# Kernel tuning notes

Measured on AMD Instinct MI355X. Metric: run time of the kernel, lower is better.

## Reference

```python
import jax, jax.numpy as jnp
import numpy as np

EMBED = 1024
HEAD = 64

def setup_inputs() -> dict:
    key = jax.random.key(0)
    k1, k2, k3, k4 = jax.random.split(key, 4)
    embeddings = jax.random.normal(k1, (8, 2048, EMBED), dtype=jnp.float32)
    # nn.Linear weight is [out, in]; we store transposed [in, out] for x @ W
    scale = 1.0 / np.sqrt(EMBED)
    Wk = jax.random.uniform(k2, (EMBED, HEAD), dtype=jnp.float32, minval=-scale, maxval=scale)
    Wq = jax.random.uniform(k3, (EMBED, HEAD), dtype=jnp.float32, minval=-scale, maxval=scale)
    Wv = jax.random.uniform(k4, (EMBED, HEAD), dtype=jnp.float32, minval=-scale, maxval=scale)
    return {"embeddings": embeddings, "Wq": Wq, "Wk": Wk, "Wv": Wv}

def reference(embeddings, Wq, Wk, Wv):
    B, S, D = embeddings.shape
    q = embeddings @ Wq  # [B,S,H]
    k = embeddings @ Wk
    v = embeddings @ Wv
    norm = k.shape[-1] ** (-0.5)
    scores = jnp.einsum('bqh,bkh->bqk', q, k) * norm  # [B,S,S]
    causal = jnp.tril(jnp.ones((S, S), dtype=bool))
    scores = jnp.where(causal, scores, -jnp.inf)
    weights = jax.nn.softmax(scores, axis=-1)
    # dropout p=0.0 (eval-equivalent): identity
    return jnp.einsum('bqk,bkh->bqh', weights, v)
```

## Files before the change

### kernel.cpp

```cpp
#include <hip/hip_runtime.h>

#define SEQ   2048
#define NBATCH 8
#define EMB   1024
#define HD    64
#define QKVSZ (NBATCH * SEQ * HD)
#define WTSZ  (3 * HD * EMB)
#define PSLOT 1088

typedef __attribute__((ext_vector_type(8))) short bf16x8;
typedef __attribute__((ext_vector_type(4))) float f32x4;

__device__ inline unsigned short f2b(float f) {
  union { float f; unsigned int i; } u; u.f = f;
  unsigned int r = (u.i + 0x7FFFu + ((u.i >> 16) & 1u)) >> 16;
  return (unsigned short)r;
}

__global__ __launch_bounds__(256) void wtrans_kernel(const float* __restrict__ wq,
                                                     const float* __restrict__ wk,
                                                     const float* __restrict__ wv,
                                                     unsigned short* __restrict__ wt) {
  int i = blockIdx.x * 256 + threadIdx.x;
  int kb  = i / 12288;
  int rem = i - kb * 12288;
  int m   = rem >> 12;
  int c   = (rem >> 6) & 63;
  int kd  = rem & 63;
  const float* src = (m == 0) ? wq : ((m == 1) ? wk : wv);
  int d = kb * 64 + kd;
  wt[i] = f2b(src[d * 64 + c]);
}

__global__ __launch_bounds__(256, 4) void qkv_proj_kernel(const float* __restrict__ emb,
                                                          const unsigned short* __restrict__ wt,
                                                          unsigned short* __restrict__ qkv) {
  __shared__ __align__(16) unsigned short Ab[2][32 * 64];
  __shared__ __align__(16) unsigned short Wb[2][96 * 64];

  const int t    = threadIdx.x;
  const int wave = t >> 6;
  const int lane = t & 63;
  const int quad = lane >> 4;
  const int l16  = lane & 15;
  const int bx = blockIdx.x;
  const int rt = bx >> 1;
  const int ch = bx & 1;
  const int wr = wave >> 1;
  const int wc = wave & 1;

  const float* aBase = emb + (size_t)rt * 32 * EMB;
  const unsigned short* wBase = wt + ch * 6144;

  f32x4 acc[3];
#pragma unroll
  for (int j = 0; j < 3; j++) acc[j] = (f32x4){0.f, 0.f, 0.f, 0.f};

  f32x4 pa[2];
  bf16x8 pw[3];

#pragma unroll
  for (int j = 0; j < 2; j++) {
    int u = t + j * 256;
    pa[j] = *(const f32x4*)(aBase + (size_t)(u >> 4) * EMB + (u & 15) * 4);
  }
#pragma unroll
  for (int j = 0; j < 3; j++) {
    int u = t + j * 256;
    pw[j] = *(const bf16x8*)(wBase + u * 8);
  }
#pragma unroll
  for (int j = 0; j < 2; j++) {
    int u = t + j * 256;
    int row = u >> 4, kq = u & 15;
    unsigned int lo = (unsigned int)f2b(pa[j][0]) | ((unsigned int)f2b(pa[j][1]) << 16);
    unsigned int hi = (unsigned int)f2b(pa[j][2]) | ((unsigned int)f2b(pa[j][3]) << 16);
    uint2 pk; pk.x = lo; pk.y = hi;
    *(uint2*)((char*)&Ab[0][0] + row * 128 + ((kq * 8) ^ ((row & 7) << 4))) = pk;
  }
#pragma unroll
  for (int j = 0; j < 3; j++) {
    int u = t + j * 256;
    int coll = u >> 3, kd8 = u & 7;
    *(bf16x8*)((char*)&Wb[0][0] + coll * 128 + ((kd8 ^ (coll & 7)) << 4)) = pw[j];
  }
  __syncthreads();

#pragma unroll 2
  for (int kb = 0; kb < 16; kb++) {
    const int cur = kb & 1;

    if (kb < 15) {
#pragma unroll
      for (int j = 0; j < 2; j++) {
        int u = t + j * 256;
        pa[j] = *(const f32x4*)(aBase + (size_t)(u >> 4) * EMB + (kb + 1) * 64 + (u & 15) * 4);
      }
#pragma unroll
      for (int j = 0; j < 3; j++) {
        int u = t + j * 256;
        pw[j] = *(const bf16x8*)(wBase + (kb + 1) * 12288 + u * 8);
      }
    }

    const int arow = wr * 16 + l16;
#pragma unroll
    for (int kh = 0; kh < 2; kh++) {
      bf16x8 af = *(const bf16x8*)((const char*)&Ab[cur][0] + arow * 128 +
                                   ((kh * 64 + quad * 16) ^ ((arow & 7) << 4)));
#pragma unroll
      for (int j = 0; j < 3; j++) {
        const int coll = (wc * 3 + j) * 16 + l16;
        bf16x8 wf = *(const bf16x8*)((const char*)&Wb[cur][0] + coll * 128 +
                                     ((kh * 64 + quad * 16) ^ ((coll & 7) << 4)));
        acc[j] = __builtin_amdgcn_mfma_f32_16x16x32_bf16(af, wf, acc[j], 0, 0, 0);
      }
    }

    if (kb < 15) {
      const int nb = cur ^ 1;
#pragma unroll
      for (int j = 0; j < 2; j++) {
        int u = t + j * 256;
        int row = u >> 4, kq = u & 15;
        unsigned int lo = (unsigned int)f2b(pa[j][0]) | ((unsigned int)f2b(pa[j][1]) << 16);
        unsigned int hi = (unsigned int)f2b(pa[j][2]) | ((unsigned int)f2b(pa[j][3]) << 16);
        uint2 pk; pk.x = lo; pk.y = hi;
        *(uint2*)((char*)&Ab[nb][0] + row * 128 + ((kq * 8) ^ ((row & 7) << 4))) = pk;
      }
#pragma unroll
      for (int j = 0; j < 3; j++) {
        int u = t + j * 256;
        int coll = u >> 3, kd8 = u & 7;
        *(bf16x8*)((char*)&Wb[nb][0] + coll * 128 + ((kd8 ^ (coll & 7)) << 4)) = pw[j];
      }
      __syncthreads();
    }
  }

#pragma unroll
  for (int j = 0; j < 3; j++) {
    int gc = ch * 96 + (wc * 3 + j) * 16 + l16;
    if (gc < 128) {
      int m  = gc >> 6, cm = gc & 63;
#pragma unroll
      for (int r = 0; r < 4; r++) {
        int row = rt * 32 + wr * 16 + quad * 4 + r;
        qkv[(size_t)m * QKVSZ + (size_t)row * HD + cm] = f2b(acc[j][r]);
      }
    }
  }

  if (ch == 1) {
    __syncthreads();
    unsigned short* Vsh = (unsigned short*)&Ab[0][0];
#pragma unroll
    for (int j = 0; j < 3; j++) {
      int gc = 96 + (wc * 3 + j) * 16 + l16;
      if (gc >= 128) {
        int h = gc - 128;
#pragma unroll
        for (int r = 0; r < 4; r++)
          Vsh[h * 40 + wr * 16 + quad * 4 + r] = f2b(acc[j][r]);
      }
    }
    __syncthreads();
    int h  = t >> 2;
    int sq = (t & 3) * 8;
    int row0 = rt * 32;
    int b    = row0 >> 11;
    int seq0 = row0 & 2047;
    bf16x8 vv = *(const bf16x8*)(Vsh + h * 40 + sq);
    *(bf16x8*)(qkv + 2 * (size_t)QKVSZ + ((size_t)(b * 64 + h)) * SEQ + seq0 + sq) = vv;
  }
}

__global__ __launch_bounds__(64, 2) void attn_split(const unsigned short* __restrict__ qkv,
                                                    float* __restrict__ part,
                                                    float* __restrict__ out) {
  __shared__ __align__(16) unsigned short Ksh[64 * 64];
  __shared__ __align__(16) unsigned short Vt[64 * 64];
  __shared__ __align__(16) unsigned short Psh[16 * 64];

  const int t = threadIdx.x;
  const int quad = t >> 4;
  const int l16  = t & 15;
  const int idx = blockIdx.x;
  const int b   = blockIdx.y;
  const int qt  = (idx < 128) ? idx : (idx - 64);
  const int c   = (idx < 128) ? 0 : 1;
  const int q0  = qt * 16;
  const int kdiag = qt >> 2;
  int t0, t1;
  if (qt < 64) { t0 = 0; t1 = kdiag; }
  else {
    int n0 = (kdiag + 2) >> 1;
    t0 = c ? n0 : 0;
    t1 = c ? kdiag : (n0 - 1);
  }

  const unsigned short* qg = qkv;
  const unsigned short* kg = qkv + QKVSZ;
  const unsigned short* vg = qkv + 2 * QKVSZ;

  const unsigned short* qptr = qg + ((size_t)(b * SEQ + q0 + l16)) * HD + quad * 8;
  const bf16x8 qf0 = *(const bf16x8*)qptr;
  const bf16x8 qf1 = *(const bf16x8*)(qptr + 32);

  f32x4 o0 = {0,0,0,0}, o1 = {0,0,0,0}, o2 = {0,0,0,0}, o3 = {0,0,0,0};
  float mst[4] = {-INFINITY, -INFINITY, -INFINITY, -INFINITY};
  float lst[4] = {0.f, 0.f, 0.f, 0.f};
  const float sc = 0.125f * 1.44269504088896f;

  bf16x8 kpre[8], vpre[8];
  {
    const unsigned short* kgb = kg + ((size_t)(b * SEQ + t0 * 64)) * HD;
#pragma unroll
    for (int i = 0; i < 8; i++) {
      int u = t + i * 64;
      kpre[i] = *(const bf16x8*)(kgb + (size_t)(u >> 3) * HD + (u & 7) * 8);
      vpre[i] = *(const bf16x8*)(vg + ((size_t)(b * 64 + (u >> 3))) * SEQ + t0 * 64 + (u & 7) * 8);
    }
  }

  for (int kb = t0; kb <= t1; kb++) {
#pragma unroll
    for (int i = 0; i < 8; i++) {
      int u = t + i * 64;
      int row = u >> 3, sb = (u & 7) * 16;
      *(bf16x8*)((char*)Ksh + row * 128 + (sb ^ ((row & 7) << 4))) = kpre[i];
      *(bf16x8*)((char*)Vt  + row * 128 + (sb ^ ((row & 7) << 4))) = vpre[i];
    }
    __syncthreads();

    if (kb < t1) {
      const unsigned short* kgb = kg + ((size_t)(b * SEQ + (kb + 1) * 64)) * HD;
#pragma unroll
      for (int i = 0; i < 8; i++) {
        int u = t + i * 64;
        kpre[i] = *(const bf16x8*)(kgb + (size_t)(u >> 3) * HD + (u & 7) * 8);
        vpre[i] = *(const bf16x8*)(vg + ((size_t)(b * 64 + (u >> 3))) * SEQ + (kb + 1) * 64 + (u & 7) * 8);
      }
    }

    f32x4 s[4];
#pragma unroll
    for (int kt = 0; kt < 4; kt++) {
      int row = kt * 16 + l16;
      bf16x8 kf0 = *(const bf16x8*)((char*)Ksh + row * 128 + ((quad * 16) ^ ((row & 7) << 4)));
      bf16x8 kf1 = *(const bf16x8*)((char*)Ksh + row * 128 + ((64 + quad * 16) ^ ((row & 7) << 4)));
      f32x4 z = {0.f, 0.f, 0.f, 0.f};
      z = __builtin_amdgcn_mfma_f32_16x16x32_bf16(qf0, kf0, z, 0, 0, 0);
      z = __builtin_amdgcn_mfma_f32_16x16x32_bf16(qf1, kf1, z, 0, 0, 0);
      s[kt] = z;
    }

    if (kb == kdiag) {
#pragma unroll
      for (int r = 0; r < 4; r++) {
        int rowg = q0 + quad * 4 + r;
#pragma unroll
        for (int kt = 0; kt < 4; kt++) {
          int col = kb * 64 + kt * 16 + l16;
          float v = s[kt][r] * sc;
          s[kt][r] = (col > rowg) ? -INFINITY : v;
        }
      }
    } else {
#pragma unroll
      for (int r = 0; r < 4; r++)
#pragma unroll
        for (int kt = 0; kt < 4; kt++) s[kt][r] *= sc;
    }

    float alpha[4];
#pragma unroll
    for (int r = 0; r < 4; r++) {
      float mx = fmaxf(fmaxf(s[0][r], s[1][r]), fmaxf(s[2][r], s[3][r]));
#pragma unroll
      for (int off = 1; off < 16; off <<= 1) mx = fmaxf(mx, __shfl_xor(mx, off, 64));
      float mnew = fmaxf(mst[r], mx);
      alpha[r] = exp2f(mst[r] - mnew);
      mst[r] = mnew;
    }
#pragma unroll
    for (int r = 0; r < 4; r++) {
      float sm = 0.f;
#pragma unroll
      for (int kt = 0; kt < 4; kt++) {
        float p = exp2f(s[kt][r] - mst[r]);
        s[kt][r] = p;
        sm += p;
      }
#pragma unroll
      for (int off = 1; off < 16; off <<= 1) sm += __shfl_xor(sm, off, 64);
      lst[r] = lst[r] * alpha[r] + sm;
    }
#pragma unroll
    for (int r = 0; r < 4; r++) { o0[r] *= alpha[r]; o1[r] *= alpha[r]; o2[r] *= alpha[r]; o3[r] *= alpha[r]; }

#pragma unroll
    for (int kt = 0; kt < 4; kt++)
#pragma unroll
      for (int r = 0; r < 4; r++) {
        int row = quad * 4 + r;
        *(unsigned short*)((char*)Psh + row * 128 + ((kt * 32 + l16 * 2) ^ ((row & 7) << 4))) = f2b(s[kt][r]);
      }
    __syncthreads();

#pragma unroll
    for (int kc = 0; kc < 2; kc++) {
      bf16x8 pf = *(const bf16x8*)((char*)Psh + l16 * 128 + ((kc * 64 + quad * 16) ^ ((l16 & 7) << 4)));
#pragma unroll
      for (int ht = 0; ht < 1; ht++) {}
      {
        int r0 = 0 * 16 + l16, r1 = 1 * 16 + l16, r2 = 2 * 16 + l16, r3 = 3 * 16 + l16;
        bf16x8 vf0 = *(const bf16x8*)((char*)Vt + r0 * 128 + ((kc * 64 + quad * 16) ^ ((r0 & 7) << 4)));
        bf16x8 vf1 = *(const bf16x8*)((char*)Vt + r1 * 128 + ((kc * 64 + quad * 16) ^ ((r1 & 7) << 4)));
        bf16x8 vf2 = *(const bf16x8*)((char*)Vt + r2 * 128 + ((kc * 64 + quad * 16) ^ ((r2 & 7) << 4)));
        bf16x8 vf3 = *(const bf16x8*)((char*)Vt + r3 * 128 + ((kc * 64 + quad * 16) ^ ((r3 & 7) << 4)));
        o0 = __builtin_amdgcn_mfma_f32_16x16x32_bf16(pf, vf0, o0, 0, 0, 0);
        o1 = __builtin_amdgcn_mfma_f32_16x16x32_bf16(pf, vf1, o1, 0, 0, 0);
        o2 = __builtin_amdgcn_mfma_f32_16x16x32_bf16(pf, vf2, o2, 0, 0, 0);
        o3 = __builtin_amdgcn_mfma_f32_16x16x32_bf16(pf, vf3, o3, 0, 0, 0);
      }
    }
    __syncthreads();
  }

  if (qt < 64) {
#pragma unroll
    for (int r = 0; r < 4; r++) {
      float inv = 1.f / lst[r];
      int rowg = q0 + quad * 4 + r;
      size_t ob = ((size_t)(b * SEQ + rowg)) * HD + l16;
      out[ob + 0]  = o0[r] * inv;
      out[ob + 16] = o1[r] * inv;
      out[ob + 32] = o2[r] * inv;
      out[ob + 48] = o3[r] * inv;
    }
  } else {
    float* ps = part + ((size_t)((b * 64 + (qt - 64)) * 2 + c)) * PSLOT;
#pragma unroll
    for (int r = 0; r < 4; r++) {
      int row = quad * 4 + r;
      ps[row * 64 + 0  + l16] = o0[r];
      ps[row * 64 + 16 + l16] = o1[r];
      ps[row * 64 + 32 + l16] = o2[r];
      ps[row * 64 + 48 + l16] = o3[r];
      if (l16 == 0) {
        ps[1024 + row] = mst[r];
        ps[1040 + row] = lst[r];
      }
    }
  }
}

__global__ __launch_bounds__(64) void attn_merge(const float* __restrict__ part,
                                                 float* __restrict__ out) {
  const int h  = threadIdx.x;
  const int qx = blockIdx.x;
  const int b  = blockIdx.y;
  const float* p0 = part + ((size_t)((b * 64 + qx) * 2 + 0)) * PSLOT;
  const float* p1 = p0 + PSLOT;
#pragma unroll 4
  for (int r = 0; r < 16; r++) {
    float m0 = p0[1024 + r], l0 = p0[1040 + r];
    float m1 = p1[1024 + r], l1 = p1[1040 + r];
    float M  = fmaxf(m0, m1);
    float e0 = exp2f(m0 - M), e1 = exp2f(m1 - M);
    float L  = l0 * e0 + l1 * e1;
    float o  = (p0[r * 64 + h] * e0 + p1[r * 64 + h] * e1) / L;
    out[((size_t)(b * SEQ + (64 + qx) * 16 + r)) * HD + h] = o;
  }
}

extern "C" void kernel_launch(void* const* d_in, const int* in_sizes, int n_in,
                              void* d_out, int out_size, void* d_ws, size_t ws_size,
                              hipStream_t stream) {
  const float* emb = (const float*)d_in[0];
  const float* wq  = (const float*)d_in[1];
  const float* wk  = (const float*)d_in[2];
  const float* wv  = (const float*)d_in[3];
  unsigned short* ws  = (unsigned short*)d_ws;
  unsigned short* wt  = ws;
  unsigned short* qkv = ws + WTSZ;
  float* part = (float*)(ws + WTSZ + 3 * QKVSZ);

  hipLaunchKernelGGL(wtrans_kernel,   dim3(WTSZ / 256), dim3(256), 0, stream, wq, wk, wv, wt);
  hipLaunchKernelGGL(qkv_proj_kernel, dim3(1024),       dim3(256), 0, stream, emb, wt, qkv);
  hipLaunchKernelGGL(attn_split,      dim3(192, 8),     dim3(64),  0, stream, qkv, part, (float*)d_out);
  hipLaunchKernelGGL(attn_merge,      dim3(64, 8),      dim3(64),  0, stream, part, (float*)d_out);
}
```

Measured before the change: 161.5 us.

## Share K/V tiles across four waves with double buffering and chunked split-K

Result: slower. 209.0 us (+29.4%).

```diff
diff --git a/kernel.cpp b/kernel.cpp
--- a/kernel.cpp
+++ b/kernel.cpp
@@ -6,7 +6,7 @@
 #define HD    64
 #define QKVSZ (NBATCH * SEQ * HD)
 #define WTSZ  (3 * HD * EMB)
-#define PSLOT 1088
+#define PSLOT2 4224
 
 typedef __attribute__((ext_vector_type(8))) short bf16x8;
 typedef __attribute__((ext_vector_type(4))) float f32x4;
@@ -175,29 +175,27 @@
   }
 }
 
-__global__ __launch_bounds__(64, 2) void attn_split(const unsigned short* __restrict__ qkv,
-                                                    float* __restrict__ part,
-                                                    float* __restrict__ out) {
-  __shared__ __align__(16) unsigned short Ksh[64 * 64];
-  __shared__ __align__(16) unsigned short Vt[64 * 64];
-  __shared__ __align__(16) unsigned short Psh[16 * 64];
-
-  const int t = threadIdx.x;
-  const int quad = t >> 4;
-  const int l16  = t & 15;
-  const int idx = blockIdx.x;
-  const int b   = blockIdx.y;
-  const int qt  = (idx < 128) ? idx : (idx - 64);
-  const int c   = (idx < 128) ? 0 : 1;
-  const int q0  = qt * 16;
-  const int kdiag = qt >> 2;
-  int t0, t1;
-  if (qt < 64) { t0 = 0; t1 = kdiag; }
-  else {
-    int n0 = (kdiag + 2) >> 1;
-    t0 = c ? n0 : 0;
-    t1 = c ? kdiag : (n0 - 1);
-  }
+__global__ __launch_bounds__(256, 4) void attn_split(const unsigned short* __restrict__ qkv,
+                                                     float* __restrict__ part,
+                                                     float* __restrict__ out) {
+  __shared__ __align__(16) unsigned short Kb[2][64 * 64];
+  __shared__ __align__(16) unsigned short Vb[2][64 * 64];
+  __shared__ __align__(16) unsigned short Pb[4][16 * 64];
+
+  const int t    = threadIdx.x;
+  const int wave = t >> 6;
+  const int lane = t & 63;
+  const int quad = lane >> 4;
+  const int l16  = lane & 15;
+  const int B0 = blockIdx.x;
+  const int c  = blockIdx.y;
+  const int b  = blockIdx.z;
+  const int nch = (B0 >> 2) + 1;
+  if (c >= nch) return;
+  const int t0 = c * 4;
+  const int t1 = min(t0 + 3, B0);
+  const int qt = B0 * 4 + wave;
+  const int q0 = qt * 16;
 
   const unsigned short* qg = qkv;
   const unsigned short* kg = qkv + QKVSZ;
@@ -212,33 +210,30 @@
   float lst[4] = {0.f, 0.f, 0.f, 0.f};
   const float sc = 0.125f * 1.44269504088896f;
 
-  bf16x8 kpre[8], vpre[8];
-  {
-    const unsigned short* kgb = kg + ((size_t)(b * SEQ + t0 * 64)) * HD;
-#pragma unroll
-    for (int i = 0; i < 8; i++) {
-      int u = t + i * 64;
-      kpre[i] = *(const bf16x8*)(kgb + (size_t)(u >> 3) * HD + (u & 7) * 8);
-      vpre[i] = *(const bf16x8*)(vg + ((size_t)(b * 64 + (u >> 3))) * SEQ + t0 * 64 + (u & 7) * 8);
-    }
-  }
+  bf16x8 kpre[2], vpre[2];
+#pragma unroll
+  for (int i = 0; i < 2; i++) {
+    int u = t + i * 256;
+    kpre[i] = *(const bf16x8*)(kg + ((size_t)(b * SEQ + t0 * 64 + (u >> 3))) * HD + (u & 7) * 8);
+    vpre[i] = *(const bf16x8*)(vg + ((size_t)(b * 64 + (u >> 3))) * SEQ + t0 * 64 + (u & 7) * 8);
+  }
+#pragma unroll
+  for (int i = 0; i < 2; i++) {
+    int u = t + i * 256;
+    int row = u >> 3, sb = (u & 7) * 16;
+    *(bf16x8*)((char*)&Kb[0][0] + row * 128 + (sb ^ ((row & 7) << 4))) = kpre[i];
+    *(bf16x8*)((char*)&Vb[0][0] + row * 128 + (sb ^ ((row & 7) << 4))) = vpre[i];
+  }
+  __syncthreads();
 
   for (int kb = t0; kb <= t1; kb++) {
-#pragma unroll
-    for (int i = 0; i < 8; i++) {
-      int u = t + i * 64;
-      int row = u >> 3, sb = (u & 7) * 16;
-      *(bf16x8*)((char*)Ksh + row * 128 + (sb ^ ((row & 7) << 4))) = kpre[i];
-      *(bf16x8*)((char*)Vt  + row * 128 + (sb ^ ((row & 7) << 4))) = vpre[i];
-    }
-    __syncthreads();
+    const int cur = (kb - t0) & 1;
 
     if (kb < t1) {
-      const unsigned short* kgb = kg + ((size_t)(b * SEQ + (kb + 1) * 64)) * HD;
-#pragma unroll
-      for (int i = 0; i < 8; i++) {
-        int u = t + i * 64;
-        kpre[i] = *(const bf16x8*)(kgb + (size_t)(u >> 3) * HD + (u & 7) * 8);
+#pragma unroll
+      for (int i = 0; i < 2; i++) {
+        int u = t + i * 256;
+        kpre[i] = *(const bf16x8*)(kg + ((size_t)(b * SEQ + (kb + 1) * 64 + (u >> 3))) * HD + (u & 7) * 8);
         vpre[i] = *(const bf16x8*)(vg + ((size_t)(b * 64 + (u >> 3))) * SEQ + (kb + 1) * 64 + (u & 7) * 8);
       }
     }
@@ -247,15 +242,15 @@
 #pragma unroll
     for (int kt = 0; kt < 4; kt++) {
       int row = kt * 16 + l16;
-      bf16x8 kf0 = *(const bf16x8*)((char*)Ksh + row * 128 + ((quad * 16) ^ ((row & 7) << 4)));
-      bf16x8 kf1 = *(const bf16x8*)((char*)Ksh + row * 128 + ((64 + quad * 16) ^ ((row & 7) << 4)));
+      bf16x8 kf0 = *(const bf16x8*)((char*)&Kb[cur][0] + row * 128 + ((quad * 16) ^ ((row & 7) << 4)));
+      bf16x8 kf1 = *(const bf16x8*)((char*)&Kb[cur][0] + row * 128 + ((64 + quad * 16) ^ ((row & 7) << 4)));
       f32x4 z = {0.f, 0.f, 0.f, 0.f};
       z = __builtin_amdgcn_mfma_f32_16x16x32_bf16(qf0, kf0, z, 0, 0, 0);
       z = __builtin_amdgcn_mfma_f32_16x16x32_bf16(qf1, kf1, z, 0, 0, 0);
       s[kt] = z;
     }
 
-    if (kb == kdiag) {
+    if (kb == B0) {
 #pragma unroll
       for (int r = 0; r < 4; r++) {
         int rowg = q0 + quad * 4 + r;
@@ -304,31 +299,39 @@
 #pragma unroll
       for (int r = 0; r < 4; r++) {
         int row = quad * 4 + r;
-        *(unsigned short*)((char*)Psh + row * 128 + ((kt * 32 + l16 * 2) ^ ((row & 7) << 4))) = f2b(s[kt][r]);
-      }
+        *(unsigned short*)((char*)&Pb[wave][0] + row * 128 +
+                           ((kt * 32 + l16 * 2) ^ ((row & 7) << 4))) = f2b(s[kt][r]);
+      }
+
+#pragma unroll
+    for (int kc = 0; kc < 2; kc++) {
+      bf16x8 pf = *(const bf16x8*)((char*)&Pb[wave][0] + l16 * 128 +
+                                   ((kc * 64 + quad * 16) ^ ((l16 & 7) << 4)));
+      int r0 = l16, r1 = 16 + l16, r2 = 32 + l16, r3 = 48 + l16;
+      bf16x8 vf0 = *(const bf16x8*)((char*)&Vb[cur][0] + r0 * 128 + ((kc * 64 + quad * 16) ^ ((r0 & 7) << 4)));
+      bf16x8 vf1 = *(const bf16x8*)((char*)&Vb[cur][0] + r1 * 128 + ((kc * 64 + quad * 16) ^ ((r1 & 7) << 4)));
+      bf16x8 vf2 = *(const bf16x8*)((char*)&Vb[cur][0] + r2 * 128 + ((kc * 64 + quad * 16) ^ ((r2 & 7) << 4)));
+      bf16x8 vf3 = *(const bf16x8*)((char*)&Vb[cur][0] + r3 * 128 + ((kc * 64 + quad * 16) ^ ((r3 & 7) << 4)));
+      o0 = __builtin_amdgcn_mfma_f32_16x16x32_bf16(pf, vf0, o0, 0, 0, 0);
+      o1 = __builtin_amdgcn_mfma_f32_16x16x32_bf16(pf, vf1, o1, 0, 0, 0);
+      o2 = __builtin_amdgcn_mfma_f32_16x16x32_bf16(pf, vf2, o2, 0, 0, 0);
+      o3 = __builtin_amdgcn_mfma_f32_16x16x32_bf16(pf, vf3, o3, 0, 0, 0);
+    }
+
+    if (kb < t1) {
+      const int nb = cur ^ 1;
+#pragma unroll
+      for (int i = 0; i < 2; i++) {
+        int u = t + i * 256;
+        int row = u >> 3, sb = (u & 7) * 16;
+        *(bf16x8*)((char*)&Kb[nb][0] + row * 128 + (sb ^ ((row & 7) << 4))) = kpre[i];
+        *(bf16x8*)((char*)&Vb[nb][0] + row * 128 + (sb ^ ((row & 7) << 4))) = vpre[i];
+      }
+    }
     __syncthreads();
-
-#pragma unroll
-    for (int kc = 0; kc < 2; kc++) {
-      bf16x8 pf = *(const bf16x8*)((char*)Psh + l16 * 128 + ((kc * 64 + quad * 16) ^ ((l16 & 7) << 4)));
-#pragma unroll
-      for (int ht = 0; ht < 1; ht++) {}
-      {
-        int r0 = 0 * 16 + l16, r1 = 1 * 16 + l16, r2 = 2 * 16 + l16, r3 = 3 * 16 + l16;
-        bf16x8 vf0 = *(const bf16x8*)((char*)Vt + r0 * 128 + ((kc * 64 + quad * 16) ^ ((r0 & 7) << 4)));
-        bf16x8 vf1 = *(const bf16x8*)((char*)Vt + r1 * 128 + ((kc * 64 + quad * 16) ^ ((r1 & 7) << 4)));
-        bf16x8 vf2 = *(const bf16x8*)((char*)Vt + r2 * 128 + ((kc * 64 + quad * 16) ^ ((r2 & 7) << 4)));
-        bf16x8 vf3 = *(const bf16x8*)((char*)Vt + r3 * 128 + ((kc * 64 + quad * 16) ^ ((r3 & 7) << 4)));
-        o0 = __builtin_amdgcn_mfma_f32_16x16x32_bf16(pf, vf0, o0, 0, 0, 0);
-        o1 = __builtin_amdgcn_mfma_f32_16x16x32_bf16(pf, vf1, o1, 0, 0, 0);
-        o2 = __builtin_amdgcn_mfma_f32_16x16x32_bf16(pf, vf2, o2, 0, 0, 0);
-        o3 = __builtin_amdgcn_mfma_f32_16x16x32_bf16(pf, vf3, o3, 0, 0, 0);
-      }
-    }
-    __syncthreads();
-  }
-
-  if (qt < 64) {
+  }
+
+  if (nch == 1) {
 #pragma unroll
     for (int r = 0; r < 4; r++) {
       float inv = 1.f / lst[r];
@@ -340,38 +343,46 @@
       out[ob + 48] = o3[r] * inv;
     }
   } else {
-    float* ps = part + ((size_t)((b * 64 + (qt - 64)) * 2 + c)) * PSLOT;
+    float* ps = part + ((size_t)((b * 32 + B0) * 8 + c)) * PSLOT2;
 #pragma unroll
     for (int r = 0; r < 4; r++) {
-      int row = quad * 4 + r;
+      int row = wave * 16 + quad * 4 + r;
       ps[row * 64 + 0  + l16] = o0[r];
       ps[row * 64 + 16 + l16] = o1[r];
       ps[row * 64 + 32 + l16] = o2[r];
       ps[row * 64 + 48 + l16] = o3[r];
       if (l16 == 0) {
-        ps[1024 + row] = mst[r];
-        ps[1040 + row] = lst[r];
-      }
-    }
-  }
-}
-
-__global__ __launch_bounds__(64) void attn_merge(const float* __restrict__ part,
-                                                 float* __restrict__ out) {
-  const int h  = threadIdx.x;
-  const int qx = blockIdx.x;
+        ps[4096 + row] = mst[r];
+        ps[4160 + row] = lst[r];
+      }
+    }
+  }
+}
+
+__global__ __launch_bounds__(256) void attn_merge(const float* __restrict__ part,
+                                                  float* __restrict__ out) {
+  const int B0 = blockIdx.x;
   const int b  = blockIdx.y;
-  const float* p0 = part + ((size_t)((b * 64 + qx) * 2 + 0)) * PSLOT;
-  const float* p1 = p0 + PSLOT;
+  const int nch = (B0 >> 2) + 1;
+  if (nch < 2) return;
+  const int t  = threadIdx.x;
+  const int h  = t & 63;
+  const int rg = t >> 6;
+  const float* base = part + ((size_t)((b * 32 + B0) * 8)) * PSLOT2;
 #pragma unroll 4
-  for (int r = 0; r < 16; r++) {
-    float m0 = p0[1024 + r], l0 = p0[1040 + r];
-    float m1 = p1[1024 + r], l1 = p1[1040 + r];
-    float M  = fmaxf(m0, m1);
-    float e0 = exp2f(m0 - M), e1 = exp2f(m1 - M);
-    float L  = l0 * e0 + l1 * e1;
-    float o  = (p0[r * 64 + h] * e0 + p1[r * 64 + h] * e1) / L;
-    out[((size_t)(b * SEQ + (64 + qx) * 16 + r)) * HD + h] = o;
+  for (int rr = 0; rr < 16; rr++) {
+    int row = rg * 16 + rr;
+    float M = -INFINITY;
+    for (int cc = 0; cc < nch; cc++)
+      M = fmaxf(M, base[(size_t)cc * PSLOT2 + 4096 + row]);
+    float L = 0.f, o = 0.f;
+    for (int cc = 0; cc < nch; cc++) {
+      const float* ps = base + (size_t)cc * PSLOT2;
+      float e = exp2f(ps[4096 + row] - M);
+      L += ps[4160 + row] * e;
+      o += ps[row * 64 + h] * e;
+    }
+    out[((size_t)(b * SEQ + B0 * 64 + row)) * HD + h] = o / L;
   }
 }
 
@@ -389,6 +400,6 @@
 
   hipLaunchKernelGGL(wtrans_kernel,   dim3(WTSZ / 256), dim3(256), 0, stream, wq, wk, wv, wt);
   hipLaunchKernelGGL(qkv_proj_kernel, dim3(1024),       dim3(256), 0, stream, emb, wt, qkv);
-  hipLaunchKernelGGL(attn_split,      dim3(192, 8),     dim3(64),  0, stream, qkv, part, (float*)d_out);
-  hipLaunchKernelGGL(attn_merge,      dim3(64, 8),      dim3(64),  0, stream, part, (float*)d_out);
-}
+  hipLaunchKernelGGL(attn_split,      dim3(32, 8, 8),   dim3(256), 0, stream, qkv, part, (float*)d_out);
+  hipLaunchKernelGGL(attn_merge,      dim3(32, 8),      dim3(256), 0, stream, part, (float*)d_out);
+}
```
